# Kernel tuning notes

Measured on AMD Instinct MI355X. Metric: run time of the kernel, lower is better.

## Reference

```python
import jax, jax.numpy as jnp
import numpy as np
import math

B, T, D = 2, 2048, 1024
H, HD = 16, 64  # n_heads, head_dim; H*HD == D

def setup_inputs() -> dict:
    key = jax.random.key(0)
    ks = jax.random.split(key, 5)
    s = 1.0 / math.sqrt(D)
    return {
        "x": jax.random.normal(ks[0], (B, T, D), dtype=jnp.float32),
        "w_qkv": jax.random.normal(ks[1], (D, 3 * D), dtype=jnp.float32) * s,
        "b_qkv": jax.random.normal(ks[2], (3 * D,), dtype=jnp.float32) * 0.01,
        "w_o": jax.random.normal(ks[3], (D, D), dtype=jnp.float32) * s,
        "b_o": jax.random.normal(ks[4], (D,), dtype=jnp.float32) * 0.01,
    }

def reference(x, w_qkv, b_qkv, w_o, b_o):
    b, t, d_model = x.shape
    qkv = x @ w_qkv + b_qkv                       # [b,t,3d]
    q, k, v = jnp.split(qkv, 3, axis=-1)
    # [b,t,d] -> [b,h,t,hd]
    q = q.reshape(b, t, H, HD).transpose(0, 2, 1, 3)
    k = k.reshape(b, t, H, HD).transpose(0, 2, 1, 3)
    v = v.reshape(b, t, H, HD).transpose(0, 2, 1, 3)
    # NOTE: original scales by sqrt(d_model), not sqrt(head_dim)
    scores = jnp.einsum('bhqd,bhkd->bhqk', q, k) / math.sqrt(d_model)
    causal = jnp.tril(jnp.ones((t, t), dtype=bool))
    scores = jnp.where(causal[None, None], scores, -jnp.inf)
    # dropout p=0.0 (pre-softmax in original) is identity
    attn = jax.nn.softmax(scores, axis=-1)
    y = jnp.einsum('bhqk,bhkd->bhqd', attn, v)    # [b,h,t,hd]
    y = y.transpose(0, 2, 1, 3).reshape(b, t, d_model)
    return y @ w_o + b_o
```

## Files before the change

### kernel.cpp

```cpp
#include <hip/hip_runtime.h>
#include <math.h>

typedef __bf16 bf16;
typedef __bf16 bf16x4 __attribute__((ext_vector_type(4)));
typedef __bf16 bf16x8 __attribute__((ext_vector_type(8)));
typedef float f32x4 __attribute__((ext_vector_type(4)));

__device__ __forceinline__ void async_copy16(const void* g, void* l) {
  __builtin_amdgcn_global_load_lds(
      (__attribute__((address_space(1))) void*)(const_cast<void*>(g)),
      (__attribute__((address_space(3))) void*)(l),
      16, 0, 0);
}

__device__ __forceinline__ void transpose_tile(
    const float* __restrict__ in, bf16* __restrict__ out, int R, int C,
    int bxi, int byi) {
  __shared__ float tile[32][33];
  int bx = bxi * 32, by = byi * 32;
  int tx = threadIdx.x & 31;
  int ty = threadIdx.x >> 5;
#pragma unroll
  for (int i = 0; i < 32; i += 8)
    tile[ty + i][tx] = in[(size_t)(by + ty + i) * C + bx + tx];
  __syncthreads();
#pragma unroll
  for (int i = 0; i < 32; i += 8)
    out[(size_t)(bx + ty + i) * R + by + tx] = (bf16)tile[tx][ty + i];
}

__global__ __launch_bounds__(256) void prep_kernel(
    const float* __restrict__ x, bf16* __restrict__ xb,
    const float* __restrict__ w_qkv, bf16* __restrict__ wqkvT,
    const float* __restrict__ w_o, bf16* __restrict__ woT) {
  int blk = blockIdx.x;
  if (blk < 4096) {
    int i = blk * 1024 + threadIdx.x * 4;
    float4 v = *(const float4*)(x + i);
    bf16x4 o;
    o[0] = (bf16)v.x; o[1] = (bf16)v.y; o[2] = (bf16)v.z; o[3] = (bf16)v.w;
    *(bf16x4*)(xb + i) = o;
  } else if (blk < 7168) {
    int tb = blk - 4096;
    transpose_tile(w_qkv, wqkvT, 1024, 3072, tb % 96, tb / 96);
  } else {
    int tb = blk - 7168;
    transpose_tile(w_o, woT, 1024, 1024, tb % 32, tb / 32);
  }
}

__device__ __forceinline__ void gemm_mainloop(
    const bf16* __restrict__ A, const bf16* __restrict__ Bt, int K,
    int bm, int bn, bf16* As, bf16* Bs, f32x4 (&acc)[4][4]) {
  int tid = threadIdx.x;
  int w = tid >> 6, lane = tid & 63;
  int wm = w & 1, wn = w >> 1;
  int col = lane & 15, quad = lane >> 4;

  int srow = w * 32 + (lane >> 2);
  int scol = (lane & 3) * 8;
  const bf16* Ag0 = A + ((size_t)(bm * 128 + srow) * K + scol);
  const bf16* Bg0 = Bt + ((size_t)(bn * 128 + srow) * K + scol);
  bf16* AsW = As + (w * 32) * 32;
  bf16* BsW = Bs + (w * 32) * 32;

  for (int k0 = 0; k0 < K; k0 += 32) {
    __syncthreads();
    async_copy16(Ag0 + k0, AsW);
    async_copy16(Ag0 + k0 + (size_t)16 * K, AsW + 16 * 32);
    async_copy16(Bg0 + k0, BsW);
    async_copy16(Bg0 + k0 + (size_t)16 * K, BsW + 16 * 32);
    __syncthreads();

    bf16x8 af[4], bfr[4];
#pragma unroll
    for (int mi = 0; mi < 4; mi++)
      af[mi] = *(const bf16x8*)(As + (wm * 64 + mi * 16 + col) * 32 + quad * 8);
#pragma unroll
    for (int ni = 0; ni < 4; ni++)
      bfr[ni] = *(const bf16x8*)(Bs + (wn * 64 + ni * 16 + col) * 32 + quad * 8);
#pragma unroll
    for (int mi = 0; mi < 4; mi++)
#pragma unroll
      for (int ni = 0; ni < 4; ni++)
        acc[mi][ni] = __builtin_amdgcn_mfma_f32_16x16x32_bf16(
            af[mi], bfr[ni], acc[mi][ni], 0, 0, 0);
  }
}

__global__ __launch_bounds__(256) void gemm_qkv_kernel(
    const bf16* __restrict__ A, const bf16* __restrict__ Bt,
    const float* __restrict__ bias, bf16* __restrict__ qb,
    bf16* __restrict__ kb, bf16* __restrict__ vtb) {
  __shared__ bf16 As[128 * 32];
  __shared__ bf16 Bs[128 * 32];
  f32x4 acc[4][4] = {};
  int bm = blockIdx.x, bn = blockIdx.y;
  gemm_mainloop(A, Bt, 1024, bm, bn, As, Bs, acc);

  int tid = threadIdx.x;
  int w = tid >> 6, lane = tid & 63;
  int wm = w & 1, wn = w >> 1;
  int col = lane & 15, quad = lane >> 4;
#pragma unroll
  for (int ni = 0; ni < 4; ni++) {
    int gc = bn * 128 + wn * 64 + ni * 16 + col;
    float bv = bias[gc];
    int which = gc >> 10;
    int dd = gc & 1023;
    int h = dd >> 6, hd = dd & 63;
    if (which == 2) {
#pragma unroll
      for (int mi = 0; mi < 4; mi++) {
        int grow0 = bm * 128 + wm * 64 + mi * 16 + quad * 4;
        int b = grow0 >> 11, t0 = grow0 & 2047;
        bf16x4 pk;
#pragma unroll
        for (int r = 0; r < 4; r++) pk[r] = (bf16)(acc[mi][ni][r] + bv);
        *(bf16x4*)&vtb[(((size_t)(b * 16 + h) * 64 + hd) * 2048) + t0] = pk;
      }
    } else {
      bf16* dst = (which == 0) ? qb : kb;
#pragma unroll
      for (int mi = 0; mi < 4; mi++) {
#pragma unroll
        for (int r = 0; r < 4; r++) {
          int grow = bm * 128 + wm * 64 + mi * 16 + quad * 4 + r;
          int b = grow >> 11, t = grow & 2047;
          dst[(((size_t)(b * 16 + h) * 2048 + t) * 64) + hd] =
              (bf16)(acc[mi][ni][r] + bv);
        }
      }
    }
  }
}

__global__ __launch_bounds__(256) void gemm_out_kernel(
    const bf16* __restrict__ A, const bf16* __restrict__ Bt,
    const float* __restrict__ bias, float* __restrict__ outp) {
  __shared__ bf16 As[128 * 32];
  __shared__ bf16 Bs[128 * 32];
  f32x4 acc[4][4] = {};
  int bm = blockIdx.x, bn = blockIdx.y;
  gemm_mainloop(A, Bt, 1024, bm, bn, As, Bs, acc);

  int tid = threadIdx.x;
  int w = tid >> 6, lane = tid & 63;
  int wm = w & 1, wn = w >> 1;
  int col = lane & 15, quad = lane >> 4;
#pragma unroll
  for (int ni = 0; ni < 4; ni++) {
    int gc = bn * 128 + wn * 64 + ni * 16 + col;
    float bv = bias[gc];
#pragma unroll
    for (int mi = 0; mi < 4; mi++) {
#pragma unroll
      for (int r = 0; r < 4; r++) {
        int grow = bm * 128 + wm * 64 + mi * 16 + quad * 4 + r;
        outp[(size_t)grow * 1024 + gc] = acc[mi][ni][r] + bv;
      }
    }
  }
}

__global__ __launch_bounds__(256, 4) void attn_kernel(
    const bf16* __restrict__ qb, const bf16* __restrict__ kb,
    const bf16* __restrict__ vtb, bf16* __restrict__ y) {
  __shared__ bf16 Ks[2][64 * 64];
  __shared__ bf16 Vs[2][64 * 64];
  __shared__ bf16 Pl[4][16][40];

  int idx = blockIdx.x;
  int qp = idx >> 5;
  int qt = (qp < 8) ? 31 - qp
           : (qp < 16) ? qp - 8
           : (qp < 24) ? 39 - qp
                       : qp - 16;
  int bh = idx & 31;
  int b = bh >> 4, h = bh & 15;
  int tid = threadIdx.x, w = tid >> 6, lane = tid & 63;
  int col = lane & 15, quad = lane >> 4;

  const bf16* Qh = qb + (size_t)bh * (2048 * 64);
  const bf16* Kh = kb + (size_t)bh * (2048 * 64);
  const bf16* Vth = vtb + (size_t)bh * (64 * 2048);

  int qrow = qt * 64 + w * 16 + col;
  bf16x8 aq[2];
#pragma unroll
  for (int ks = 0; ks < 2; ks++) {
    aq[ks] = *(const bf16x8*)(Qh + (size_t)qrow * 64 + ks * 32 + quad * 8);
#pragma unroll
    for (int e = 0; e < 8; e++)
      aq[ks][e] = (bf16)((float)aq[ks][e] * 0.03125f);
  }

  int r0 = w * 16 + (lane >> 3);
  int r1 = r0 + 8;
  int ch0 = (lane & 7) ^ (r0 & 7);
  int ch1 = (lane & 7) ^ (r1 & 7);
  size_t koff0 = (size_t)r0 * 64 + ch0 * 8;
  size_t koff1 = (size_t)r1 * 64 + ch1 * 8;
  size_t voff0 = (size_t)r0 * 2048 + ch0 * 8;
  size_t voff1 = (size_t)r1 * 2048 + ch1 * 8;
  int lw0 = (w * 16) * 64;
  int lw1 = (w * 16 + 8) * 64;

  float l_part = 0.f;
  f32x4 ot[4] = {};
  int qglob = qt * 64 + w * 16 + col;

  auto stage = [&](int j, int buf) {
    const bf16* Kt = Kh + (size_t)j * 64 * 64;
    const bf16* Vt_ = Vth + (size_t)j * 64;
    async_copy16(Kt + koff0, Ks[buf] + lw0);
    async_copy16(Kt + koff1, Ks[buf] + lw1);
    async_copy16(Vt_ + voff0, Vs[buf] + lw0);
    async_copy16(Vt_ + voff1, Vs[buf] + lw1);
  };

  auto tile_compute = [&](int j, int buf, bool diag) {
    const bf16* Ksb = Ks[buf];
    const bf16* Vsb = Vs[buf];
    f32x4 st[4] = {};
#pragma unroll
    for (int ks = 0; ks < 2; ks++)
#pragma unroll
      for (int c = 0; c < 4; c++) {
        int t = c * 16 + col;
        int slot = t * 8 + (((ks << 2) + quad) ^ (t & 7));
        bf16x8 ak = *(const bf16x8*)(Ksb + slot * 8);
        st[c] = __builtin_amdgcn_mfma_f32_16x16x32_bf16(ak, aq[ks], st[c],
                                                        0, 0, 0);
      }
#pragma unroll
    for (int half = 0; half < 2; half++) {
#pragma unroll
      for (int cc = 0; cc < 2; cc++) {
        int c = half * 2 + cc;
        bf16x4 pk;
#pragma unroll
        for (int r = 0; r < 4; r++) {
          int tglob = j * 64 + c * 16 + quad * 4 + r;
          float pv = (diag && tglob > qglob) ? 0.f : __expf(st[c][r]);
          l_part += pv;
          pk[r] = (bf16)pv;
        }
        *(bf16x4*)&Pl[w][col][cc * 16 + quad * 4] = pk;
      }
      __builtin_amdgcn_sched_barrier(0);
      __builtin_amdgcn_s_waitcnt(0xc07f);
      __builtin_amdgcn_sched_barrier(0);
      bf16x8 ap = *(const bf16x8*)&Pl[w][col][quad * 8];
#pragma unroll
      for (int c = 0; c < 4; c++) {
        int d = c * 16 + col;
        int slot = d * 8 + (((half << 2) + quad) ^ (d & 7));
        bf16x8 av = *(const bf16x8*)(Vsb + slot * 8);
        ot[c] = __builtin_amdgcn_mfma_f32_16x16x32_bf16(av, ap, ot[c],
                                                        0, 0, 0);
      }
    }
  };

  int j = 0;
  for (; j < qt; j += 2) {
    __syncthreads();
    stage(j, 0);
    stage(j + 1, 1);
    __syncthreads();
    tile_compute(j, 0, false);
    tile_compute(j + 1, 1, j + 1 == qt);
  }
  if (j == qt) {
    __syncthreads();
    stage(j, 0);
    __syncthreads();
    tile_compute(j, 0, true);
  }

  float sum = l_part;
  sum += __shfl_xor(sum, 16, 64);
  sum += __shfl_xor(sum, 32, 64);
  float inv = 1.f / sum;
  int tq = qt * 64 + w * 16 + col;
  bf16* yrow = y + ((size_t)(b * 2048 + tq)) * 1024 + h * 64;
#pragma unroll
  for (int c = 0; c < 4; c++) {
    bf16x4 pk;
#pragma unroll
    for (int r = 0; r < 4; r++) pk[r] = (bf16)(ot[c][r] * inv);
    *(bf16x4*)(yrow + c * 16 + quad * 4) = pk;
  }
}

extern "C" void kernel_launch(void* const* d_in, const int* in_sizes, int n_in,
                              void* d_out, int out_size, void* d_ws,
                              size_t ws_size, hipStream_t stream) {
  const float* x = (const float*)d_in[0];
  const float* w_qkv = (const float*)d_in[1];
  const float* b_qkv = (const float*)d_in[2];
  const float* w_o = (const float*)d_in[3];
  const float* b_o = (const float*)d_in[4];
  float* out = (float*)d_out;

  char* p = (char*)d_ws;
  bf16* xb    = (bf16*)p; p += (size_t)4096 * 1024 * 2;
  bf16* wqkvT = (bf16*)p; p += (size_t)3072 * 1024 * 2;
  bf16* woT   = (bf16*)p; p += (size_t)1024 * 1024 * 2;
  bf16* qb    = (bf16*)p; p += (size_t)2 * 16 * 2048 * 64 * 2;
  bf16* kb    = (bf16*)p; p += (size_t)2 * 16 * 2048 * 64 * 2;
  bf16* vtb   = (bf16*)p; p += (size_t)2 * 16 * 64 * 2048 * 2;
  bf16* yb    = (bf16*)p; p += (size_t)4096 * 1024 * 2;

  prep_kernel<<<8192, 256, 0, stream>>>(x, xb, w_qkv, wqkvT, w_o, woT);
  gemm_qkv_kernel<<<dim3(32, 24), 256, 0, stream>>>(
      xb, wqkvT, b_qkv, qb, kb, vtb);
  attn_kernel<<<1024, 256, 0, stream>>>(qb, kb, vtb, yb);
  gemm_out_kernel<<<dim3(32, 8), 256, 0, stream>>>(yb, woT, b_o, out);
}
```

Measured before the change: 169.9 us.

## Deepen GEMM K-tile to 64 with XOR-swizzled LDS and vectorized epilogue

The shared GEMM mainloop now stages 64-wide K tiles, which halves the number of barrier pairs per K loop. LDS chunks are placed with an XOR swizzle so the fragment reads avoid bank conflicts. MFMA operands are swapped so each lane holds four consecutive output columns, which lets the epilogues use float4 bias loads and vector bf16x4/float4 stores for Q, K and the output. The trade-off is doubled LDS per block, and the V-transpose stores become scalar.

```diff
diff --git a/kernel.cpp b/kernel.cpp
--- a/kernel.cpp
+++ b/kernel.cpp
@@ -49,7 +49,7 @@
   }
 }
 
-__device__ __forceinline__ void gemm_mainloop(
+__device__ __forceinline__ void gemm_mainloop64(
     const bf16* __restrict__ A, const bf16* __restrict__ Bt, int K,
     int bm, int bn, bf16* As, bf16* Bs, f32x4 (&acc)[4][4]) {
   int tid = threadIdx.x;
@@ -57,34 +57,43 @@
   int wm = w & 1, wn = w >> 1;
   int col = lane & 15, quad = lane >> 4;
 
-  int srow = w * 32 + (lane >> 2);
-  int scol = (lane & 3) * 8;
-  const bf16* Ag0 = A + ((size_t)(bm * 128 + srow) * K + scol);
-  const bf16* Bg0 = Bt + ((size_t)(bn * 128 + srow) * K + scol);
-  bf16* AsW = As + (w * 32) * 32;
-  bf16* BsW = Bs + (w * 32) * 32;
-
-  for (int k0 = 0; k0 < K; k0 += 32) {
-    __syncthreads();
-    async_copy16(Ag0 + k0, AsW);
-    async_copy16(Ag0 + k0 + (size_t)16 * K, AsW + 16 * 32);
-    async_copy16(Bg0 + k0, BsW);
-    async_copy16(Bg0 + k0 + (size_t)16 * K, BsW + 16 * 32);
-    __syncthreads();
-
-    bf16x8 af[4], bfr[4];
-#pragma unroll
-    for (int mi = 0; mi < 4; mi++)
-      af[mi] = *(const bf16x8*)(As + (wm * 64 + mi * 16 + col) * 32 + quad * 8);
-#pragma unroll
-    for (int ni = 0; ni < 4; ni++)
-      bfr[ni] = *(const bf16x8*)(Bs + (wn * 64 + ni * 16 + col) * 32 + quad * 8);
-#pragma unroll
-    for (int mi = 0; mi < 4; mi++)
-#pragma unroll
-      for (int ni = 0; ni < 4; ni++)
-        acc[mi][ni] = __builtin_amdgcn_mfma_f32_16x16x32_bf16(
-            af[mi], bfr[ni], acc[mi][ni], 0, 0, 0);
+  int srow = w * 32 + (lane >> 3);
+
+  for (int k0 = 0; k0 < K; k0 += 64) {
+    __syncthreads();
+#pragma unroll
+    for (int c = 0; c < 4; c++) {
+      int r = srow + c * 8;
+      int ch = (lane & 7) ^ (r & 7);
+      async_copy16(A + (size_t)(bm * 128 + r) * K + k0 + ch * 8,
+                   As + (w * 32 + c * 8) * 64);
+      async_copy16(Bt + (size_t)(bn * 128 + r) * K + k0 + ch * 8,
+                   Bs + (w * 32 + c * 8) * 64);
+    }
+    __syncthreads();
+
+#pragma unroll
+    for (int ks = 0; ks < 2; ks++) {
+      bf16x8 af[4], bfr[4];
+#pragma unroll
+      for (int mi = 0; mi < 4; mi++) {
+        int m = wm * 64 + mi * 16 + col;
+        af[mi] =
+            *(const bf16x8*)(As + m * 64 + ((((ks << 2) + quad)) ^ (m & 7)) * 8);
+      }
+#pragma unroll
+      for (int ni = 0; ni < 4; ni++) {
+        int n = wn * 64 + ni * 16 + col;
+        bfr[ni] =
+            *(const bf16x8*)(Bs + n * 64 + ((((ks << 2) + quad)) ^ (n & 7)) * 8);
+      }
+#pragma unroll
+      for (int mi = 0; mi < 4; mi++)
+#pragma unroll
+        for (int ni = 0; ni < 4; ni++)
+          acc[mi][ni] = __builtin_amdgcn_mfma_f32_16x16x32_bf16(
+              bfr[ni], af[mi], acc[mi][ni], 0, 0, 0);
+    }
   }
 }
 
@@ -92,44 +101,47 @@
     const bf16* __restrict__ A, const bf16* __restrict__ Bt,
     const float* __restrict__ bias, bf16* __restrict__ qb,
     bf16* __restrict__ kb, bf16* __restrict__ vtb) {
-  __shared__ bf16 As[128 * 32];
-  __shared__ bf16 Bs[128 * 32];
+  __shared__ bf16 As[128 * 64];
+  __shared__ bf16 Bs[128 * 64];
   f32x4 acc[4][4] = {};
   int bm = blockIdx.x, bn = blockIdx.y;
-  gemm_mainloop(A, Bt, 1024, bm, bn, As, Bs, acc);
+  gemm_mainloop64(A, Bt, 1024, bm, bn, As, Bs, acc);
 
   int tid = threadIdx.x;
   int w = tid >> 6, lane = tid & 63;
   int wm = w & 1, wn = w >> 1;
   int col = lane & 15, quad = lane >> 4;
+
 #pragma unroll
   for (int ni = 0; ni < 4; ni++) {
-    int gc = bn * 128 + wn * 64 + ni * 16 + col;
-    float bv = bias[gc];
-    int which = gc >> 10;
-    int dd = gc & 1023;
-    int h = dd >> 6, hd = dd & 63;
+    int f0 = bn * 128 + wn * 64 + ni * 16 + quad * 4;
+    float4 b4 = *(const float4*)(bias + f0);
+    int which = f0 >> 10;
+    int dd = f0 & 1023;
+    int h = dd >> 6, hd0 = dd & 63;
     if (which == 2) {
 #pragma unroll
       for (int mi = 0; mi < 4; mi++) {
-        int grow0 = bm * 128 + wm * 64 + mi * 16 + quad * 4;
-        int b = grow0 >> 11, t0 = grow0 & 2047;
-        bf16x4 pk;
-#pragma unroll
-        for (int r = 0; r < 4; r++) pk[r] = (bf16)(acc[mi][ni][r] + bv);
-        *(bf16x4*)&vtb[(((size_t)(b * 16 + h) * 64 + hd) * 2048) + t0] = pk;
+        int tok = bm * 128 + wm * 64 + mi * 16 + col;
+        int b = tok >> 11, t = tok & 2047;
+        size_t base = ((size_t)(b * 16 + h) * 64 + hd0) * 2048 + t;
+        vtb[base] = (bf16)(acc[mi][ni][0] + b4.x);
+        vtb[base + 2048] = (bf16)(acc[mi][ni][1] + b4.y);
+        vtb[base + 4096] = (bf16)(acc[mi][ni][2] + b4.z);
+        vtb[base + 6144] = (bf16)(acc[mi][ni][3] + b4.w);
       }
     } else {
       bf16* dst = (which == 0) ? qb : kb;
 #pragma unroll
       for (int mi = 0; mi < 4; mi++) {
-#pragma unroll
-        for (int r = 0; r < 4; r++) {
-          int grow = bm * 128 + wm * 64 + mi * 16 + quad * 4 + r;
-          int b = grow >> 11, t = grow & 2047;
-          dst[(((size_t)(b * 16 + h) * 2048 + t) * 64) + hd] =
-              (bf16)(acc[mi][ni][r] + bv);
-        }
+        int tok = bm * 128 + wm * 64 + mi * 16 + col;
+        int b = tok >> 11, t = tok & 2047;
+        bf16x4 pk;
+        pk[0] = (bf16)(acc[mi][ni][0] + b4.x);
+        pk[1] = (bf16)(acc[mi][ni][1] + b4.y);
+        pk[2] = (bf16)(acc[mi][ni][2] + b4.z);
+        pk[3] = (bf16)(acc[mi][ni][3] + b4.w);
+        *(bf16x4*)&dst[((size_t)(b * 16 + h) * 2048 + t) * 64 + hd0] = pk;
       }
     }
   }
@@ -138,27 +150,30 @@
 __global__ __launch_bounds__(256) void gemm_out_kernel(
     const bf16* __restrict__ A, const bf16* __restrict__ Bt,
     const float* __restrict__ bias, float* __restrict__ outp) {
-  __shared__ bf16 As[128 * 32];
-  __shared__ bf16 Bs[128 * 32];
+  __shared__ bf16 As[128 * 64];
+  __shared__ bf16 Bs[128 * 64];
   f32x4 acc[4][4] = {};
   int bm = blockIdx.x, bn = blockIdx.y;
-  gemm_mainloop(A, Bt, 1024, bm, bn, As, Bs, acc);
+  gemm_mainloop64(A, Bt, 1024, bm, bn, As, Bs, acc);
 
   int tid = threadIdx.x;
   int w = tid >> 6, lane = tid & 63;
   int wm = w & 1, wn = w >> 1;
   int col = lane & 15, quad = lane >> 4;
+
 #pragma unroll
   for (int ni = 0; ni < 4; ni++) {
-    int gc = bn * 128 + wn * 64 + ni * 16 + col;
-    float bv = bias[gc];
+    int f0 = bn * 128 + wn * 64 + ni * 16 + quad * 4;
+    float4 b4 = *(const float4*)(bias + f0);
 #pragma unroll
     for (int mi = 0; mi < 4; mi++) {
-#pragma unroll
-      for (int r = 0; r < 4; r++) {
-        int grow = bm * 128 + wm * 64 + mi * 16 + quad * 4 + r;
-        outp[(size_t)grow * 1024 + gc] = acc[mi][ni][r] + bv;
-      }
+      int tok = bm * 128 + wm * 64 + mi * 16 + col;
+      float4 ov;
+      ov.x = acc[mi][ni][0] + b4.x;
+      ov.y = acc[mi][ni][1] + b4.y;
+      ov.z = acc[mi][ni][2] + b4.z;
+      ov.w = acc[mi][ni][3] + b4.w;
+      *(float4*)(outp + (size_t)tok * 1024 + f0) = ov;
     }
   }
 }
```

New measurement: 179.5 us. 5.7% more time.
